# Kernel tuning notes

Measured on AMD Instinct MI355X. Metric: run time of the kernel, lower is better.

The kernel has to match this reference:

```python
import jax, jax.numpy as jnp
import numpy as np
from itertools import permutations

B, Nm, S, K, H, OUT = 32, 128, 16, 4, 128, 1
LG, LI, LGL = 3, 2, 2  # num_layer, num_layer_id, num_layer_global
EPS = 1e-5


def _ln(x, g, b):
    m = jnp.mean(x, -1, keepdims=True)
    v = jnp.mean(jnp.square(x - m), -1, keepdims=True)
    return (x - m) * jax.lax.rsqrt(v + EPS) * g + b


def _block(x, W1, b1, W2, b2, g, bn):
    # Linear -> ReLU -> Linear -> LayerNorm -> ReLU
    h = jax.nn.relu(x @ W1 + b1)
    return jax.nn.relu(_ln(h @ W2 + b2, g, bn))


def setup_inputs() -> dict:
    key = jax.random.key(0)
    ks = iter(jax.random.split(key, 64))
    nrm = lambda shape, s=0.05: jax.random.normal(next(ks), shape, jnp.float32) * s
    x = nrm((B, Nm, 1), 1.0)
    adj = (jax.random.uniform(next(ks), (B, Nm, Nm)) < 0.05).astype(jnp.float32)
    # allperm: all permutations of [1..K-1] with 0 prepended, transposed -> (K, permdim)
    ap = np.array(list(permutations(range(1, K))), dtype=np.int32)
    ap = np.concatenate([np.zeros((ap.shape[0], 1), np.int32), ap], axis=1).T
    allperm = jnp.asarray(ap)
    Ssub = B * S
    base = jax.random.randint(next(ks), (Ssub,), 0, Nm - K)
    subgs = base[:, None] + jnp.arange(K, dtype=jnp.int32)[None, :]  # distinct nodes per subgraph
    num_subg = jnp.full((B,), S, jnp.int32)
    num_node = jnp.full((B,), Nm, jnp.int32)
    d = dict(x=x, adj=adj,
             idemb=nrm((K + 2, H)),
             in_W1=nrm((1, H)), in_b1=jnp.zeros((H,)), in_W2=nrm((H, H)), in_b2=jnp.zeros((H,)),
             in_g=jnp.ones((H,)), in_bn=jnp.zeros((H,)),
             gW1=nrm((LG, H, H)), gb1=jnp.zeros((LG, H)), gW2=nrm((LG, H, H)), gb2=jnp.zeros((LG, H)),
             gg=jnp.ones((LG, H)), gbn=jnp.zeros((LG, H)),
             iW1=nrm((LI, H, H)), ib1=jnp.zeros((LI, H)), iW2=nrm((LI, H, H)), ib2=jnp.zeros((LI, H)),
             ig=jnp.ones((LI, H)), ibn=jnp.zeros((LI, H)),
             glW1=nrm((LGL, H, H)), glb1=jnp.zeros((LGL, H)), glW2=nrm((LGL, H, H)), glb2=jnp.zeros((LGL, H)),
             glg=jnp.ones((LGL, H)), glbn=jnp.zeros((LGL, H)),
             s1_W=nrm((H, H)), s1_b=jnp.zeros((H,)), s2_W=nrm((H, H)), s2_b=jnp.zeros((H,)),
             rW1=nrm((H, H)), rb1=jnp.zeros((H,)), rW2=nrm((H, H)), rb2=jnp.zeros((H,)),
             rg=jnp.ones((H,)), rbn=jnp.zeros((H,)),
             out_W=nrm((H, OUT)), out_b=jnp.zeros((OUT,)),
             subgs=subgs, num_subg=num_subg, num_node=num_node, allperm=allperm)
    return d


def reference(x, adj, idemb, in_W1, in_b1, in_W2, in_b2, in_g, in_bn,
              gW1, gb1, gW2, gb2, gg, gbn,
              iW1, ib1, iW2, ib2, ig, ibn,
              glW1, glb1, glW2, glb2, glg, glbn,
              s1_W, s1_b, s2_W, s2_b,
              rW1, rb1, rW2, rb2, rg, rbn,
              out_W, out_b, subgs, num_subg, num_node, allperm):
    Bsz, N = x.shape[0], x.shape[1]
    Ssub, k = subgs.shape
    permdim = allperm.shape[1]
    # input embedding MLP
    h = _block(x, in_W1, in_b1, in_W2, in_b2, in_g, in_bn)  # (B, Nm, H)
    Hd = h.shape[-1]
    # subgraph -> graph batch map (ns_b = S per graph; Ssub static)
    subgbatch = jnp.repeat(jnp.arange(Bsz), num_subg, total_repeat_length=Ssub)
    # identity labeling: z starts as ones, labeled nodes get idemb(allperm[pos])
    lb = jnp.repeat(jnp.arange(Ssub), k)          # label batch (subgraph idx)
    lnodes = subgs.reshape(-1)                    # node ids within graph
    ni = jnp.tile(jnp.arange(k), Ssub)            # position within subgraph
    vals = idemb[allperm[ni]]                     # (Ssub*k, permdim, H)
    z = jnp.ones((Ssub, N, permdim, Hd), x.dtype)
    z = z.at[lb, lnodes].multiply(vals)
    # graph message passing on full graphs
    for l in range(gW1.shape[0]):
        m = jnp.einsum('bij,bjd->bid', adj, h)
        h = h + _block(m, gW1[l], gb1[l], gW2[l], gb2[l], gg[l], gbn[l])
    hs = h[subgbatch]        # (Ssub, Nm, H)
    sadj = adj[subgbatch]    # (Ssub, Nm, Nm)
    # id message passing over permutation channels
    for l in range(iW1.shape[0]):
        m = jnp.einsum('bij,bjpd->bipd', sadj, z)
        z = z + _block(m, iW1[l], ib1[l], iW2[l], ib2[l], ig[l], ibn[l])
    # zero out padded (null) nodes
    null_mask = jnp.arange(N)[None, :] >= num_node[:, None]  # (B, Nm)
    z = jnp.where(null_mask[subgbatch][:, :, None, None], 0.0, z)
    z = jax.nn.relu(z.mean(axis=2) @ s1_W + s1_b)  # setmlp1, (Ssub, Nm, H)
    hs = hs + z
    for l in range(glW1.shape[0]):
        m = jnp.einsum('bij,bjd->bid', sadj, hs)
        hs = hs + _block(m, glW1[l], glb1[l], glW2[l], glb2[l], glg[l], glbn[l])
    hs = jax.nn.relu(hs.sum(axis=1) @ s2_W + s2_b)  # setmlp2, (Ssub, H)
    pooled = jax.ops.segment_max(hs, subgbatch, num_segments=Bsz)  # global max pool
    pooled = pooled + _block(pooled, rW1, rb1, rW2, rb2, rg, rbn)  # setmlp3 (1 layer)
    return pooled @ out_W + out_b  # (B, OUT)
```

## Files before the change

### kernel.cpp

```cpp
#include <hip/hip_runtime.h>
#include <hip/hip_bf16.h>
#include <string.h>

typedef __hip_bfloat16 bf16;
typedef short v8s __attribute__((ext_vector_type(8)));
typedef float v4f __attribute__((ext_vector_type(4)));

#define H_ 128
#define P_ 6
#define K_ 4
#define NBR_CAP 48

__device__ __forceinline__ float ldf(const float* p, size_t i) { return p[i]; }
__device__ __forceinline__ float ldf(const bf16* p, size_t i) { return __bfloat162float(p[i]); }

__device__ __forceinline__ float s2f(short s) {
    unsigned int u = ((unsigned int)(unsigned short)s) << 16;
    float f; __builtin_memcpy(&f, &u, 4); return f;
}
__device__ __forceinline__ short f2s(float v) {
    bf16 h = __float2bfloat16(v);
    short s; __builtin_memcpy(&s, &h, 2); return s;
}
__device__ __forceinline__ v4f MFMA(v8s a, v8s b, v4f c) {
    return __builtin_amdgcn_mfma_f32_16x16x32_bf16(a, b, c, 0, 0, 0);
}

__global__ __launch_bounds__(128) void k_csr(const float* __restrict__ adj,
    unsigned char* __restrict__ nbr, int* __restrict__ deg, float* __restrict__ degf)
{
    const int gi = blockIdx.x * 128 + threadIdx.x;
    const float* row = adj + (size_t)gi * 128;
    unsigned char* nb = nbr + (size_t)gi * NBR_CAP;
    int c = 0; float s = 0.f;
    for (int j = 0; j < 128; ++j) {
        float a = row[j];
        if (a != 0.f) { s += a; if (c < NBR_CAP) nb[c] = (unsigned char)j; ++c; }
    }
    deg[gi] = (c < NBR_CAP) ? c : NBR_CAP;
    degf[gi] = s;
}

__global__ __launch_bounds__(128) void k_adjb(const float* __restrict__ adj, bf16* __restrict__ adjb)
{
    const size_t i = (size_t)blockIdx.x * 128 + threadIdx.x;
    adjb[i] = __float2bfloat16(adj[i]);
}

__global__ __launch_bounds__(128) void k_wt8(
    const float* s0, const float* s1, const float* s2, const float* s3,
    const float* s4, const float* s5, const float* s6, const float* s7,
    bf16* __restrict__ dst)
{
    const int w = blockIdx.x >> 7, n = blockIdx.x & 127, k = threadIdx.x;
    const float* arr[8] = {s0, s1, s2, s3, s4, s5, s6, s7};
    dst[(size_t)w * 16384 + n * 128 + k] = __float2bfloat16(arr[w][k * 128 + n]);
}

__global__ __launch_bounds__(128) void k_wt1(const float* __restrict__ src, bf16* __restrict__ dst)
{
    const int n = blockIdx.x, k = threadIdx.x;
    dst[n * 128 + k] = __float2bfloat16(src[k * 128 + n]);
}

__global__ __launch_bounds__(128) void k_in_t1(const float* __restrict__ x,
    const float* __restrict__ W1, const float* __restrict__ b1, float* __restrict__ t1)
{
    int r = blockIdx.x, hd = threadIdx.x;
    t1[(size_t)r * H_ + hd] = fmaxf(fmaf(x[r], W1[hd], b1[hd]), 0.f);
}

template<bool DO_MM1, bool HAS_RES>
__global__ __launch_bounds__(128) void k_block(
    const float* __restrict__ in, const float* __restrict__ res, float* __restrict__ out,
    const float* __restrict__ W1, const float* __restrict__ b1,
    const float* __restrict__ W2, const float* __restrict__ b2,
    const float* __restrict__ gam, const float* __restrict__ bet)
{
    __shared__ float sA[16][136];
    __shared__ float sB[16][136];
    __shared__ float sStat[32];
    const int hd = threadIdx.x;
    const size_t row0 = (size_t)blockIdx.x * 16;
    #pragma unroll
    for (int r = 0; r < 16; ++r) sA[r][hd] = in[(row0 + r) * H_ + hd];
    __syncthreads();
    float acc[16];
    if (DO_MM1) {
        #pragma unroll
        for (int r = 0; r < 16; ++r) acc[r] = b1[hd];
        for (int k = 0; k < H_; k += 4) {
            float w0 = W1[(k+0)*H_+hd], w1 = W1[(k+1)*H_+hd], w2 = W1[(k+2)*H_+hd], w3 = W1[(k+3)*H_+hd];
            #pragma unroll
            for (int r = 0; r < 16; ++r) {
                float4 a = *(const float4*)&sA[r][k];
                acc[r] = fmaf(a.x, w0, acc[r]); acc[r] = fmaf(a.y, w1, acc[r]);
                acc[r] = fmaf(a.z, w2, acc[r]); acc[r] = fmaf(a.w, w3, acc[r]);
            }
        }
        #pragma unroll
        for (int r = 0; r < 16; ++r) sB[r][hd] = fmaxf(acc[r], 0.f);
    } else {
        #pragma unroll
        for (int r = 0; r < 16; ++r) sB[r][hd] = sA[r][hd];
    }
    __syncthreads();
    #pragma unroll
    for (int r = 0; r < 16; ++r) acc[r] = b2[hd];
    for (int k = 0; k < H_; k += 4) {
        float w0 = W2[(k+0)*H_+hd], w1 = W2[(k+1)*H_+hd], w2 = W2[(k+2)*H_+hd], w3 = W2[(k+3)*H_+hd];
        #pragma unroll
        for (int r = 0; r < 16; ++r) {
            float4 a = *(const float4*)&sB[r][k];
            acc[r] = fmaf(a.x, w0, acc[r]); acc[r] = fmaf(a.y, w1, acc[r]);
            acc[r] = fmaf(a.z, w2, acc[r]); acc[r] = fmaf(a.w, w3, acc[r]);
        }
    }
    __syncthreads();
    #pragma unroll
    for (int r = 0; r < 16; ++r) sA[r][hd] = acc[r];
    __syncthreads();
    if (hd < 16) {
        float s = 0.f, ss = 0.f;
        for (int k = 0; k < H_; ++k) { float v = sA[hd][k]; s += v; ss += v * v; }
        float mean = s * (1.f / H_);
        float var = ss * (1.f / H_) - mean * mean;
        sStat[hd] = mean; sStat[16 + hd] = rsqrtf(var + 1e-5f);
    }
    __syncthreads();
    float gv = gam[hd], bv = bet[hd];
    #pragma unroll
    for (int r = 0; r < 16; ++r) {
        float v = fmaxf((acc[r] - sStat[r]) * sStat[16 + r] * gv + bv, 0.f);
        if (HAS_RES) v += res[(row0 + r) * H_ + hd];
        out[(row0 + r) * H_ + hd] = v;
    }
}

template<bool GATHER, typename T>
__global__ __launch_bounds__(128) void k_gemm_relu(
    const T* __restrict__ in, const float* __restrict__ res, float* __restrict__ out,
    const float* __restrict__ W, const float* __restrict__ b)
{
    __shared__ float sA[16][136];
    const int hd = threadIdx.x;
    const size_t row0 = (size_t)blockIdx.x * 16;
    #pragma unroll
    for (int r = 0; r < 16; ++r) sA[r][hd] = ldf(in, (row0 + r) * H_ + hd);
    __syncthreads();
    float acc[16];
    #pragma unroll
    for (int r = 0; r < 16; ++r) acc[r] = b[hd];
    for (int k = 0; k < H_; k += 4) {
        float w0 = W[(k+0)*H_+hd], w1 = W[(k+1)*H_+hd], w2 = W[(k+2)*H_+hd], w3 = W[(k+3)*H_+hd];
        #pragma unroll
        for (int r = 0; r < 16; ++r) {
            float4 a = *(const float4*)&sA[r][k];
            acc[r] = fmaf(a.x, w0, acc[r]); acc[r] = fmaf(a.y, w1, acc[r]);
            acc[r] = fmaf(a.z, w2, acc[r]); acc[r] = fmaf(a.w, w3, acc[r]);
        }
    }
    #pragma unroll
    for (int r = 0; r < 16; ++r) {
        size_t rr = row0 + r;
        float v = fmaxf(acc[r], 0.f);
        if (GATHER) {
            int i = (int)(rr & 127);
            int g = (int)(rr >> 11);
            v += res[((size_t)(g * 128 + i)) * H_ + hd];
        }
        out[rr * H_ + hd] = v;
    }
}

__global__ __launch_bounds__(128) void k_spmv(const float* __restrict__ adj,
    const float* __restrict__ xin, float* __restrict__ mout, int subShift)
{
    __shared__ float sAdj[128];
    const int hd = threadIdx.x;
    const int bi = blockIdx.x;
    const int bb = bi >> 7, i = bi & 127;
    const int g = bb >> subShift;
    sAdj[hd] = adj[((size_t)(g * 128 + i)) * 128 + hd];
    __syncthreads();
    float acc = 0.f;
    const float* xb = xin + (size_t)bb * 128 * H_ + hd;
    for (int j = 0; j < 128; ++j) {
        float a = sAdj[j];
        if (a != 0.f) acc = fmaf(a, xb[(size_t)j * H_], acc);
    }
    mout[(size_t)bi * H_ + hd] = acc;
}

__global__ __launch_bounds__(256) void k_id1_fused(
    const float* __restrict__ adj, const float* __restrict__ degf,
    const int* __restrict__ subgs, const int* __restrict__ allperm,
    const float* __restrict__ idemb, bf16* __restrict__ outb,
    const bf16* __restrict__ W1t, const float* __restrict__ b1,
    const bf16* __restrict__ W2t, const float* __restrict__ b2,
    const float* __restrict__ gam, const float* __restrict__ bet)
{
    __shared__ __align__(16) short sIn[128][136];
    __shared__ __align__(16) short tb[4][32][136];
    __shared__ float sE[K_][128];
    const int t = threadIdx.x;
    const int bi = blockIdx.x;
    const int b_s = bi / 6, p = bi - b_s * 6;
    const int g = b_s >> 4;
    const int wave = t >> 6, lane = t & 63;
    const int quad = lane >> 4, l16 = lane & 15;

    int nodeq[K_];
    #pragma unroll
    for (int q = 0; q < K_; ++q) nodeq[q] = subgs[b_s * K_ + q];

    for (int u = t; u < K_ * 128; u += 256) {
        const int q = u >> 7, f = u & 127;
        sE[q][f] = idemb[(size_t)allperm[q * P_ + p] * H_ + f] - 1.f;
    }
    __syncthreads();

    {
        const int i = t >> 1, half = (t & 1) * 64;
        const int gi = g * 128 + i;
        const float dg = degf[gi];
        float aq[K_];
        #pragma unroll
        for (int q = 0; q < K_; ++q) aq[q] = adj[(size_t)gi * 128 + nodeq[q]];
        #pragma unroll
        for (int f = 0; f < 64; ++f) {
            float v = dg;
            #pragma unroll
            for (int q = 0; q < K_; ++q) v = fmaf(aq[q], sE[q][half + f], v);
            sIn[i][half + f] = f2s(v);
        }
    }
    __syncthreads();

    v4f acc[2][8];
    #pragma unroll
    for (int mt = 0; mt < 2; ++mt)
        #pragma unroll
        for (int nt = 0; nt < 8; ++nt) acc[mt][nt] = (v4f){0.f, 0.f, 0.f, 0.f};
    #pragma unroll
    for (int kk = 0; kk < 4; ++kk) {
        v8s a0 = *(const v8s*)&sIn[wave * 32 + l16][kk * 32 + quad * 8];
        v8s a1 = *(const v8s*)&sIn[wave * 32 + 16 + l16][kk * 32 + quad * 8];
        #pragma unroll
        for (int nt = 0; nt < 8; ++nt) {
            v8s b = *(const v8s*)(W1t + (nt * 16 + l16) * 128 + kk * 32 + quad * 8);
            acc[0][nt] = MFMA(a0, b, acc[0][nt]);
            acc[1][nt] = MFMA(a1, b, acc[1][nt]);
        }
    }
    #pragma unroll
    for (int nt = 0; nt < 8; ++nt) {
        float bb = b1[nt * 16 + l16];
        #pragma unroll
        for (int mt = 0; mt < 2; ++mt)
            #pragma unroll
            for (int r = 0; r < 4; ++r)
                tb[wave][mt * 16 + quad * 4 + r][nt * 16 + l16] = f2s(fmaxf(acc[mt][nt][r] + bb, 0.f));
    }
    #pragma unroll
    for (int mt = 0; mt < 2; ++mt)
        #pragma unroll
        for (int nt = 0; nt < 8; ++nt) acc[mt][nt] = (v4f){0.f, 0.f, 0.f, 0.f};
    #pragma unroll
    for (int kk = 0; kk < 4; ++kk) {
        v8s a0 = *(const v8s*)&tb[wave][l16][kk * 32 + quad * 8];
        v8s a1 = *(const v8s*)&tb[wave][16 + l16][kk * 32 + quad * 8];
        #pragma unroll
        for (int nt = 0; nt < 8; ++nt) {
            v8s b = *(const v8s*)(W2t + (nt * 16 + l16) * 128 + kk * 32 + quad * 8);
            acc[0][nt] = MFMA(a0, b, acc[0][nt]);
            acc[1][nt] = MFMA(a1, b, acc[1][nt]);
        }
    }
    float bb2[8], gv[8], bv[8];
    #pragma unroll
    for (int nt = 0; nt < 8; ++nt) {
        int n = nt * 16 + l16;
        bb2[nt] = b2[n]; gv[nt] = gam[n]; bv[nt] = bet[n];
    }
    #pragma unroll
    for (int mt = 0; mt < 2; ++mt)
        #pragma unroll
        for (int r = 0; r < 4; ++r) {
            float s = 0.f, q = 0.f;
            #pragma unroll
            for (int nt = 0; nt < 8; ++nt) {
                float u = acc[mt][nt][r] + bb2[nt];
                acc[mt][nt][r] = u;
                s += u; q += u * u;
            }
            #pragma unroll
            for (int d = 1; d < 16; d <<= 1) {
                s += __shfl_xor(s, d);
                q += __shfl_xor(q, d);
            }
            float mn = s * (1.f / 128.f);
            float rs = rsqrtf(q * (1.f / 128.f) - mn * mn + 1e-5f);
            #pragma unroll
            for (int nt = 0; nt < 8; ++nt) {
                float v = fmaxf((acc[mt][nt][r] - mn) * rs * gv[nt] + bv[nt], 0.f);
                tb[wave][mt * 16 + quad * 4 + r][nt * 16 + l16] = f2s(v + 1.0f);
            }
        }
    __syncthreads();
    {
        const int f = t >> 1, nh = (t & 1) * 64;
        const short* flat = &tb[0][0][0];
        bf16* dst = outb + (size_t)bi * 16384 + (size_t)f * 128 + nh;
        #pragma unroll
        for (int u = 0; u < 8; ++u) {
            v8s pk;
            #pragma unroll
            for (int e = 0; e < 8; ++e) pk[e] = flat[(nh + u * 8 + e) * 136 + f];
            *(v8s*)(dst + u * 8) = pk;
        }
    }
}

__global__ __launch_bounds__(256) void k_id2_v9(
    const bf16* __restrict__ z2t, bf16* __restrict__ zm,
    const bf16* __restrict__ adjb, const int* __restrict__ num_node,
    const int* __restrict__ subgs, const int* __restrict__ allperm,
    const float* __restrict__ idemb,
    const bf16* __restrict__ W1t, const float* __restrict__ b1,
    const bf16* __restrict__ W2t, const float* __restrict__ b2,
    const float* __restrict__ gam, const float* __restrict__ bet)
{
    __shared__ __align__(16) short sB[128][136];
    __shared__ float sP[4][128];
    const int t = threadIdx.x;
    const int b_s = blockIdx.x;
    const int g = b_s >> 4;
    const int wave = t >> 6, lane = t & 63, quad = lane >> 4, l16 = lane & 15;
    const int wrow = wave << 5;

    #pragma unroll
    for (int u = 0; u < 2; ++u) {
        const int v = t + u * 256;
        const int a = v >> 7, n = v & 127;
        const float* src = (a == 0) ? b1 : (a == 1) ? b2 : (a == 2) ? gam : bet;
        sP[a][n] = src[n];
    }

    v8s aA[2][4];
    {
        const bf16* ar = adjb + (size_t)g * 16384;
        #pragma unroll
        for (int mt = 0; mt < 2; ++mt)
            #pragma unroll
            for (int kk = 0; kk < 4; ++kk)
                aA[mt][kk] = *(const v8s*)(ar + (size_t)(wrow + mt * 16 + l16) * 128 + kk * 32 + quad * 8);
    }
    int nodeq[K_];
    #pragma unroll
    for (int q = 0; q < K_; ++q) nodeq[q] = subgs[b_s * K_ + q];

    float macc[2][8][4];
    #pragma unroll
    for (int mt = 0; mt < 2; ++mt)
        #pragma unroll
        for (int nt = 0; nt < 8; ++nt)
            #pragma unroll
            for (int r = 0; r < 4; ++r) macc[mt][nt][r] = 0.f;

    const int sf = t >> 1, shalf = (t & 1) * 64;

    for (int p = 0; p < P_; ++p) {
        {
            const bf16* src = z2t + ((size_t)(b_s * P_ + p)) * 16384 + (size_t)sf * 128 + shalf;
            #pragma unroll
            for (int u = 0; u < 8; ++u)
                *(v8s*)&sB[sf][shalf + u * 8] = *(const v8s*)(src + u * 8);
        }
        __syncthreads();
        if (t < 128) {
            #pragma unroll
            for (int q = 0; q < K_; ++q) {
                float e = idemb[(size_t)allperm[q * P_ + p] * H_ + t] - 1.f;
                short* cell = &sB[t][nodeq[q]];
                *cell = f2s(s2f(*cell) + e);
            }
        }
        __syncthreads();
        #pragma unroll
        for (int mt = 0; mt < 2; ++mt)
            #pragma unroll
            for (int nt = 0; nt < 8; ++nt) {
                const int n = nt * 16 + l16;
                #pragma unroll
                for (int r = 0; r < 4; ++r)
                    macc[mt][nt][r] += s2f(sB[n][wrow + mt * 16 + quad * 4 + r]);
            }
        v4f acc[2][8];
        #pragma unroll
        for (int mt = 0; mt < 2; ++mt)
            #pragma unroll
            for (int nt = 0; nt < 8; ++nt) acc[mt][nt] = (v4f){0.f, 0.f, 0.f, 0.f};
        #pragma unroll
        for (int kk = 0; kk < 4; ++kk)
            #pragma unroll
            for (int nt = 0; nt < 8; ++nt) {
                v8s b = *(const v8s*)&sB[nt * 16 + l16][kk * 32 + quad * 8];
                acc[0][nt] = MFMA(aA[0][kk], b, acc[0][nt]);
                acc[1][nt] = MFMA(aA[1][kk], b, acc[1][nt]);
            }
        __syncthreads();
        #pragma unroll
        for (int nt = 0; nt < 8; ++nt)
            #pragma unroll
            for (int mt = 0; mt < 2; ++mt)
                #pragma unroll
                for (int r = 0; r < 4; ++r)
                    sB[wrow + mt * 16 + quad * 4 + r][nt * 16 + l16] = f2s(acc[mt][nt][r]);
        #pragma unroll
        for (int mt = 0; mt < 2; ++mt)
            #pragma unroll
            for (int nt = 0; nt < 8; ++nt) acc[mt][nt] = (v4f){0.f, 0.f, 0.f, 0.f};
        #pragma unroll
        for (int kk = 0; kk < 4; ++kk) {
            v8s a0 = *(const v8s*)&sB[wrow + l16][kk * 32 + quad * 8];
            v8s a1 = *(const v8s*)&sB[wrow + 16 + l16][kk * 32 + quad * 8];
            #pragma unroll
            for (int nt = 0; nt < 8; ++nt) {
                v8s b = *(const v8s*)(W1t + (nt * 16 + l16) * 128 + kk * 32 + quad * 8);
                acc[0][nt] = MFMA(a0, b, acc[0][nt]);
                acc[1][nt] = MFMA(a1, b, acc[1][nt]);
            }
        }
        #pragma unroll
        for (int nt = 0; nt < 8; ++nt) {
            float bb = sP[0][nt * 16 + l16];
            #pragma unroll
            for (int mt = 0; mt < 2; ++mt)
                #pragma unroll
                for (int r = 0; r < 4; ++r)
                    sB[wrow + mt * 16 + quad * 4 + r][nt * 16 + l16] = f2s(fmaxf(acc[mt][nt][r] + bb, 0.f));
        }
        #pragma unroll
        for (int mt = 0; mt < 2; ++mt)
            #pragma unroll
            for (int nt = 0; nt < 8; ++nt) acc[mt][nt] = (v4f){0.f, 0.f, 0.f, 0.f};
        #pragma unroll
        for (int kk = 0; kk < 4; ++kk) {
            v8s a0 = *(const v8s*)&sB[wrow + l16][kk * 32 + quad * 8];
            v8s a1 = *(const v8s*)&sB[wrow + 16 + l16][kk * 32 + quad * 8];
            #pragma unroll
            for (int nt = 0; nt < 8; ++nt) {
                v8s b = *(const v8s*)(W2t + (nt * 16 + l16) * 128 + kk * 32 + quad * 8);
                acc[0][nt] = MFMA(a0, b, acc[0][nt]);
                acc[1][nt] = MFMA(a1, b, acc[1][nt]);
            }
        }
        #pragma unroll
        for (int mt = 0; mt < 2; ++mt)
            #pragma unroll
            for (int r = 0; r < 4; ++r) {
                float s = 0.f, qq = 0.f;
                #pragma unroll
                for (int nt = 0; nt < 8; ++nt) {
                    float u = acc[mt][nt][r] + sP[1][nt * 16 + l16];
                    acc[mt][nt][r] = u;
                    s += u; qq += u * u;
                }
                #pragma unroll
                for (int d = 1; d < 16; d <<= 1) {
                    s += __shfl_xor(s, d);
                    qq += __shfl_xor(qq, d);
                }
                float mn = s * (1.f / 128.f);
                float rs = rsqrtf(qq * (1.f / 128.f) - mn * mn + 1e-5f);
                #pragma unroll
                for (int nt = 0; nt < 8; ++nt) {
                    const int n = nt * 16 + l16;
                    macc[mt][nt][r] += fmaxf((acc[mt][nt][r] - mn) * rs * sP[2][n] + sP[3][n], 0.f);
                }
            }
        __syncthreads();
    }
    const int nn = num_node[g];
    #pragma unroll
    for (int mt = 0; mt < 2; ++mt)
        #pragma unroll
        for (int nt = 0; nt < 8; ++nt)
            #pragma unroll
            for (int r = 0; r < 4; ++r) {
                const int i = wrow + mt * 16 + quad * 4 + r;
                const int n = nt * 16 + l16;
                float v = (i >= nn) ? 0.f : macc[mt][nt][r] * (1.f / 6.f);
                zm[((size_t)(b_s * 128 + i)) * 128 + n] = __float2bfloat16(v);
            }
}

__global__ __launch_bounds__(256) void k_gl_fused(
    const bf16* __restrict__ zm, const float* __restrict__ hb,
    const bf16* __restrict__ adjb,
    const bf16* __restrict__ s1Wt, const float* __restrict__ s1_b,
    const bf16* __restrict__ WTgl,
    const float* __restrict__ glb1, const float* __restrict__ glb2,
    const float* __restrict__ glg, const float* __restrict__ glbn,
    float* __restrict__ hsum)
{
    __shared__ __align__(16) short sHsT[128][136];
    __shared__ __align__(16) short sM[128][136];
    __shared__ float sP[9][128];
    const int t = threadIdx.x;
    const int b_s = blockIdx.x;
    const int g = b_s >> 4;
    const int wave = t >> 6, lane = t & 63, quad = lane >> 4, l16 = lane & 15;
    const int wrow = wave << 5;

    for (int u = t; u < 9 * 128; u += 256) {
        const int a = u >> 7, n = u & 127;
        const float* src =
            (a == 0) ? glb1 : (a == 1) ? glb2 : (a == 2) ? glg : (a == 3) ? glbn :
            (a == 4) ? glb1 + 128 : (a == 5) ? glb2 + 128 : (a == 6) ? glg + 128 :
            (a == 7) ? glbn + 128 : s1_b;
        sP[a][n] = src[n];
    }

    v8s aA[2][4];
    {
        const bf16* ar = adjb + (size_t)g * 16384;
        #pragma unroll
        for (int mt = 0; mt < 2; ++mt)
            #pragma unroll
            for (int kk = 0; kk < 4; ++kk)
                aA[mt][kk] = *(const v8s*)(ar + (size_t)(wrow + mt * 16 + l16) * 128 + kk * 32 + quad * 8);
    }

    v4f acc[2][8];
    #pragma unroll
    for (int mt = 0; mt < 2; ++mt)
        #pragma unroll
        for (int nt = 0; nt < 8; ++nt) acc[mt][nt] = (v4f){0.f, 0.f, 0.f, 0.f};
    #pragma unroll
    for (int kk = 0; kk < 4; ++kk) {
        v8s a0 = *(const v8s*)(zm + ((size_t)(b_s * 128) + wrow + l16) * 128 + kk * 32 + quad * 8);
        v8s a1 = *(const v8s*)(zm + ((size_t)(b_s * 128) + wrow + 16 + l16) * 128 + kk * 32 + quad * 8);
        #pragma unroll
        for (int nt = 0; nt < 8; ++nt) {
            v8s b = *(const v8s*)(s1Wt + (nt * 16 + l16) * 128 + kk * 32 + quad * 8);
            acc[0][nt] = MFMA(a0, b, acc[0][nt]);
            acc[1][nt] = MFMA(a1, b, acc[1][nt]);
        }
    }
    __syncthreads();
    float hs_reg[2][8][4];
    #pragma unroll
    for (int mt = 0; mt < 2; ++mt)
        #pragma unroll
        for (int nt = 0; nt < 8; ++nt)
            #pragma unroll
            for (int r = 0; r < 4; ++r) {
                const int i = wrow + mt * 16 + quad * 4 + r;
                const int n = nt * 16 + l16;
                float v = fmaxf(acc[mt][nt][r] + sP[8][n], 0.f);
                v += hb[((size_t)(g * 128 + i)) * 128 + n];
                hs_reg[mt][nt][r] = v;
                sHsT[n][i] = f2s(v);
            }
    __syncthreads();

    for (int l = 0; l < 2; ++l) {
        const bf16* W1t = WTgl + (size_t)(2 * l) * 16384;
        const bf16* W2t = WTgl + (size_t)(2 * l + 1) * 16384;
        #pragma unroll
        for (int mt = 0; mt < 2; ++mt)
            #pragma unroll
            for (int nt = 0; nt < 8; ++nt) acc[mt][nt] = (v4f){0.f, 0.f, 0.f, 0.f};
        #pragma unroll
        for (int kk = 0; kk < 4; ++kk)
            #pragma unroll
            for (int nt = 0; nt < 8; ++nt) {
                v8s b = *(const v8s*)&sHsT[nt * 16 + l16][kk * 32 + quad * 8];
                acc[0][nt] = MFMA(aA[0][kk], b, acc[0][nt]);
                acc[1][nt] = MFMA(aA[1][kk], b, acc[1][nt]);
            }
        #pragma unroll
        for (int nt = 0; nt < 8; ++nt)
            #pragma unroll
            for (int mt = 0; mt < 2; ++mt)
                #pragma unroll
                for (int r = 0; r < 4; ++r)
                    sM[wrow + mt * 16 + quad * 4 + r][nt * 16 + l16] = f2s(acc[mt][nt][r]);
        __syncthreads();
        #pragma unroll
        for (int mt = 0; mt < 2; ++mt)
            #pragma unroll
            for (int nt = 0; nt < 8; ++nt) acc[mt][nt] = (v4f){0.f, 0.f, 0.f, 0.f};
        #pragma unroll
        for (int kk = 0; kk < 4; ++kk) {
            v8s a0 = *(const v8s*)&sM[wrow + l16][kk * 32 + quad * 8];
            v8s a1 = *(const v8s*)&sM[wrow + 16 + l16][kk * 32 + quad * 8];
            #pragma unroll
            for (int nt = 0; nt < 8; ++nt) {
                v8s b = *(const v8s*)(W1t + (nt * 16 + l16) * 128 + kk * 32 + quad * 8);
                acc[0][nt] = MFMA(a0, b, acc[0][nt]);
                acc[1][nt] = MFMA(a1, b, acc[1][nt]);
            }
        }
        #pragma unroll
        for (int nt = 0; nt < 8; ++nt) {
            float bb = sP[4 * l + 0][nt * 16 + l16];
            #pragma unroll
            for (int mt = 0; mt < 2; ++mt)
                #pragma unroll
                for (int r = 0; r < 4; ++r)
                    sM[wrow + mt * 16 + quad * 4 + r][nt * 16 + l16] = f2s(fmaxf(acc[mt][nt][r] + bb, 0.f));
        }
        #pragma unroll
        for (int mt = 0; mt < 2; ++mt)
            #pragma unroll
            for (int nt = 0; nt < 8; ++nt) acc[mt][nt] = (v4f){0.f, 0.f, 0.f, 0.f};
        #pragma unroll
        for (int kk = 0; kk < 4; ++kk) {
            v8s a0 = *(const v8s*)&sM[wrow + l16][kk * 32 + quad * 8];
            v8s a1 = *(const v8s*)&sM[wrow + 16 + l16][kk * 32 + quad * 8];
            #pragma unroll
            for (int nt = 0; nt < 8; ++nt) {
                v8s b = *(const v8s*)(W2t + (nt * 16 + l16) * 128 + kk * 32 + quad * 8);
                acc[0][nt] = MFMA(a0, b, acc[0][nt]);
                acc[1][nt] = MFMA(a1, b, acc[1][nt]);
            }
        }
        #pragma unroll
        for (int mt = 0; mt < 2; ++mt)
            #pragma unroll
            for (int r = 0; r < 4; ++r) {
                float s = 0.f, qq = 0.f;
                #pragma unroll
                for (int nt = 0; nt < 8; ++nt) {
                    float u = acc[mt][nt][r] + sP[4 * l + 1][nt * 16 + l16];
                    acc[mt][nt][r] = u;
                    s += u; qq += u * u;
                }
                #pragma unroll
                for (int d = 1; d < 16; d <<= 1) {
                    s += __shfl_xor(s, d);
                    qq += __shfl_xor(qq, d);
                }
                float mn = s * (1.f / 128.f);
                float rs = rsqrtf(qq * (1.f / 128.f) - mn * mn + 1e-5f);
                const int i = wrow + mt * 16 + quad * 4 + r;
                #pragma unroll
                for (int nt = 0; nt < 8; ++nt) {
                    const int n = nt * 16 + l16;
                    float v = fmaxf((acc[mt][nt][r] - mn) * rs * sP[4 * l + 2][n] + sP[4 * l + 3][n], 0.f);
                    float h2 = hs_reg[mt][nt][r] + v;
                    hs_reg[mt][nt][r] = h2;
                    sHsT[n][i] = f2s(h2);
                }
            }
        __syncthreads();
    }

    float* sRedf = (float*)&sM[0][0];
    #pragma unroll
    for (int nt = 0; nt < 8; ++nt) {
        float part = 0.f;
        #pragma unroll
        for (int mt = 0; mt < 2; ++mt)
            #pragma unroll
            for (int r = 0; r < 4; ++r) part += hs_reg[mt][nt][r];
        sRedf[(wave * 4 + quad) * 128 + nt * 16 + l16] = part;
    }
    __syncthreads();
    if (t < 128) {
        float s = 0.f;
        #pragma unroll
        for (int r = 0; r < 16; ++r) s += sRedf[r * 128 + t];
        hsum[(size_t)b_s * 128 + t] = s;
    }
}

__global__ __launch_bounds__(128) void k_maxpool(const float* __restrict__ hs2, float* __restrict__ pooled)
{
    const int g = blockIdx.x, hd = threadIdx.x;
    float m = -INFINITY;
    for (int s = 0; s < 16; ++s) m = fmaxf(m, hs2[((size_t)(g * 16 + s)) * H_ + hd]);
    pooled[(size_t)g * H_ + hd] = m;
}

__global__ __launch_bounds__(128) void k_out(const float* __restrict__ pooled2,
    const float* __restrict__ out_W, const float* __restrict__ out_b, float* __restrict__ out)
{
    __shared__ float red[128];
    const int g = blockIdx.x, hd = threadIdx.x;
    red[hd] = pooled2[(size_t)g * H_ + hd] * out_W[hd];
    __syncthreads();
    for (int s = 64; s > 0; s >>= 1) {
        if (hd < s) red[hd] += red[hd + s];
        __syncthreads();
    }
    if (hd == 0) out[g] = red[0] + out_b[0];
}

extern "C" void kernel_launch(void* const* d_in, const int* in_sizes, int n_in,
                              void* d_out, int out_size, void* d_ws, size_t ws_size,
                              hipStream_t stream)
{
    (void)in_sizes; (void)n_in; (void)out_size; (void)ws_size;
    const float* x     = (const float*)d_in[0];
    const float* adj   = (const float*)d_in[1];
    const float* idemb = (const float*)d_in[2];
    const float* in_W1 = (const float*)d_in[3];
    const float* in_b1 = (const float*)d_in[4];
    const float* in_W2 = (const float*)d_in[5];
    const float* in_b2 = (const float*)d_in[6];
    const float* in_g  = (const float*)d_in[7];
    const float* in_bn = (const float*)d_in[8];
    const float* gW1   = (const float*)d_in[9];
    const float* gb1   = (const float*)d_in[10];
    const float* gW2   = (const float*)d_in[11];
    const float* gb2   = (const float*)d_in[12];
    const float* gg    = (const float*)d_in[13];
    const float* gbn   = (const float*)d_in[14];
    const float* iW1   = (const float*)d_in[15];
    const float* ib1   = (const float*)d_in[16];
    const float* iW2   = (const float*)d_in[17];
    const float* ib2   = (const float*)d_in[18];
    const float* ig    = (const float*)d_in[19];
    const float* ibn   = (const float*)d_in[20];
    const float* glW1  = (const float*)d_in[21];
    const float* glb1  = (const float*)d_in[22];
    const float* glW2  = (const float*)d_in[23];
    const float* glb2  = (const float*)d_in[24];
    const float* glg   = (const float*)d_in[25];
    const float* glbn  = (const float*)d_in[26];
    const float* s1_W  = (const float*)d_in[27];
    const float* s1_b  = (const float*)d_in[28];
    const float* s2_W  = (const float*)d_in[29];
    const float* s2_b  = (const float*)d_in[30];
    const float* rW1   = (const float*)d_in[31];
    const float* rb1   = (const float*)d_in[32];
    const float* rW2   = (const float*)d_in[33];
    const float* rb2   = (const float*)d_in[34];
    const float* rg    = (const float*)d_in[35];
    const float* rbn   = (const float*)d_in[36];
    const float* out_W = (const float*)d_in[37];
    const float* out_b = (const float*)d_in[38];
    const int* subgs   = (const int*)d_in[39];
    const int* num_node= (const int*)d_in[41];
    const int* allperm = (const int*)d_in[42];

    const size_t MB_ = (size_t)512 * 128 * P_ * H_ * 2;
    char* w = (char*)d_ws;
    bf16*  mz     = (bf16*)(w);
    bf16*  s1Wt   = (bf16*)(w + 33554432ull);
    bf16*  zm     = (bf16*)(w + MB_);
    bf16*  WT     = (bf16*)(w + MB_ + 16777216ull);
    char*  wc     = w + MB_ + 16777216ull + 262144ull;
    float* hb     = (float*)(wc);
    float* sb2    = (float*)(wc + 2097152ull);
    bf16*  adjb   = (bf16*)(wc + 2097152ull);
    float* hsum   = (float*)(wc + 4194304ull);
    float* hs2    = (float*)(wc + 4456448ull);
    float* pooled = (float*)(wc + 4718592ull);
    float* pooled2= (float*)(wc + 4734976ull);
    unsigned char* nbr = (unsigned char*)(wc + 4751360ull);
    int*   deg    = (int*)(wc + 4947968ull);
    float* degf   = (float*)(wc + 4964352ull);
    float* outp   = (float*)d_out;

    k_csr<<<32, 128, 0, stream>>>(adj, nbr, deg, degf);
    k_wt8<<<1024, 128, 0, stream>>>(iW1, iW2, iW1 + 16384, iW2 + 16384,
                                    glW1, glW2, glW1 + 16384, glW2 + 16384, WT);

    k_in_t1<<<4096, 128, 0, stream>>>(x, in_W1, in_b1, sb2);
    k_block<false, false><<<256, 128, 0, stream>>>(sb2, nullptr, hb,
        nullptr, nullptr, in_W2, in_b2, in_g, in_bn);

    for (int l = 0; l < 3; ++l) {
        k_spmv<<<4096, 128, 0, stream>>>(adj, hb, sb2, 0);
        k_block<true, true><<<256, 128, 0, stream>>>(sb2, hb, hb,
            gW1 + l * 16384, gb1 + l * 128, gW2 + l * 16384, gb2 + l * 128,
            gg + l * 128, gbn + l * 128);
    }

    k_adjb<<<4096, 128, 0, stream>>>(adj, adjb);

    k_id1_fused<<<3072, 256, 0, stream>>>(adj, degf, subgs, allperm, idemb, mz,
        WT, ib1, WT + 16384, ib2, ig, ibn);

    k_id2_v9<<<512, 256, 0, stream>>>(mz, zm, adjb, num_node, subgs, allperm, idemb,
        WT + 2 * 16384, ib1 + 128, WT + 3 * 16384, ib2 + 128, ig + 128, ibn + 128);

    k_wt1<<<128, 128, 0, stream>>>(s1_W, s1Wt);

    k_gl_fused<<<512, 256, 0, stream>>>(zm, hb, adjb, s1Wt, s1_b,
        WT + 4 * 16384, glb1, glb2, glg, glbn, hsum);

    k_gemm_relu<false, float><<<32, 128, 0, stream>>>(hsum, nullptr, hs2, s2_W, s2_b);
    k_maxpool<<<32, 128, 0, stream>>>(hs2, pooled);
    k_block<true, true><<<2, 128, 0, stream>>>(pooled, pooled, pooled2,
        rW1, rb1, rW2, rb2, rg, rbn);
    k_out<<<32, 128, 0, stream>>>(pooled2, out_W, out_b, outp);
}
```

Measured before the change: 685.6 us.

## Fuse id-layer-1 and id-layer-2 kernels to keep permutation activations on-chip

Merges the first id message-passing layer kernel into the second, so each subgraph block computes the layer-1 input, both MLP GEMMs and layernorm per permutation, then writes the transposed result into shared memory for layer 2. This removes a large bf16 intermediate buffer (about 100MB written and read back) and one kernel launch. In exchange, grid parallelism drops from 3072 to 512 blocks with a serial loop over six permutations, and each block does more work and synchronisation.

```diff
diff --git a/kernel.cpp b/kernel.cpp
--- a/kernel.cpp
+++ b/kernel.cpp
@@ -4,6 +4,7 @@
 
 typedef __hip_bfloat16 bf16;
 typedef short v8s __attribute__((ext_vector_type(8)));
+typedef short v4s __attribute__((ext_vector_type(4)));
 typedef float v4f __attribute__((ext_vector_type(4)));
 
 #define H_ 128
@@ -192,147 +193,18 @@
     mout[(size_t)bi * H_ + hd] = acc;
 }
 
-__global__ __launch_bounds__(256) void k_id1_fused(
+__global__ __launch_bounds__(256) void k_id12(
     const float* __restrict__ adj, const float* __restrict__ degf,
-    const int* __restrict__ subgs, const int* __restrict__ allperm,
-    const float* __restrict__ idemb, bf16* __restrict__ outb,
-    const bf16* __restrict__ W1t, const float* __restrict__ b1,
-    const bf16* __restrict__ W2t, const float* __restrict__ b2,
-    const float* __restrict__ gam, const float* __restrict__ bet)
-{
-    __shared__ __align__(16) short sIn[128][136];
-    __shared__ __align__(16) short tb[4][32][136];
-    __shared__ float sE[K_][128];
-    const int t = threadIdx.x;
-    const int bi = blockIdx.x;
-    const int b_s = bi / 6, p = bi - b_s * 6;
-    const int g = b_s >> 4;
-    const int wave = t >> 6, lane = t & 63;
-    const int quad = lane >> 4, l16 = lane & 15;
-
-    int nodeq[K_];
-    #pragma unroll
-    for (int q = 0; q < K_; ++q) nodeq[q] = subgs[b_s * K_ + q];
-
-    for (int u = t; u < K_ * 128; u += 256) {
-        const int q = u >> 7, f = u & 127;
-        sE[q][f] = idemb[(size_t)allperm[q * P_ + p] * H_ + f] - 1.f;
-    }
-    __syncthreads();
-
-    {
-        const int i = t >> 1, half = (t & 1) * 64;
-        const int gi = g * 128 + i;
-        const float dg = degf[gi];
-        float aq[K_];
-        #pragma unroll
-        for (int q = 0; q < K_; ++q) aq[q] = adj[(size_t)gi * 128 + nodeq[q]];
-        #pragma unroll
-        for (int f = 0; f < 64; ++f) {
-            float v = dg;
-            #pragma unroll
-            for (int q = 0; q < K_; ++q) v = fmaf(aq[q], sE[q][half + f], v);
-            sIn[i][half + f] = f2s(v);
-        }
-    }
-    __syncthreads();
-
-    v4f acc[2][8];
-    #pragma unroll
-    for (int mt = 0; mt < 2; ++mt)
-        #pragma unroll
-        for (int nt = 0; nt < 8; ++nt) acc[mt][nt] = (v4f){0.f, 0.f, 0.f, 0.f};
-    #pragma unroll
-    for (int kk = 0; kk < 4; ++kk) {
-        v8s a0 = *(const v8s*)&sIn[wave * 32 + l16][kk * 32 + quad * 8];
-        v8s a1 = *(const v8s*)&sIn[wave * 32 + 16 + l16][kk * 32 + quad * 8];
-        #pragma unroll
-        for (int nt = 0; nt < 8; ++nt) {
-            v8s b = *(const v8s*)(W1t + (nt * 16 + l16) * 128 + kk * 32 + quad * 8);
-            acc[0][nt] = MFMA(a0, b, acc[0][nt]);
-            acc[1][nt] = MFMA(a1, b, acc[1][nt]);
-        }
-    }
-    #pragma unroll
-    for (int nt = 0; nt < 8; ++nt) {
-        float bb = b1[nt * 16 + l16];
-        #pragma unroll
-        for (int mt = 0; mt < 2; ++mt)
-            #pragma unroll
-            for (int r = 0; r < 4; ++r)
-                tb[wave][mt * 16 + quad * 4 + r][nt * 16 + l16] = f2s(fmaxf(acc[mt][nt][r] + bb, 0.f));
-    }
-    #pragma unroll
-    for (int mt = 0; mt < 2; ++mt)
-        #pragma unroll
-        for (int nt = 0; nt < 8; ++nt) acc[mt][nt] = (v4f){0.f, 0.f, 0.f, 0.f};
-    #pragma unroll
-    for (int kk = 0; kk < 4; ++kk) {
-        v8s a0 = *(const v8s*)&tb[wave][l16][kk * 32 + quad * 8];
-        v8s a1 = *(const v8s*)&tb[wave][16 + l16][kk * 32 + quad * 8];
-        #pragma unroll
-        for (int nt = 0; nt < 8; ++nt) {
-            v8s b = *(const v8s*)(W2t + (nt * 16 + l16) * 128 + kk * 32 + quad * 8);
-            acc[0][nt] = MFMA(a0, b, acc[0][nt]);
-            acc[1][nt] = MFMA(a1, b, acc[1][nt]);
-        }
-    }
-    float bb2[8], gv[8], bv[8];
-    #pragma unroll
-    for (int nt = 0; nt < 8; ++nt) {
-        int n = nt * 16 + l16;
-        bb2[nt] = b2[n]; gv[nt] = gam[n]; bv[nt] = bet[n];
-    }
-    #pragma unroll
-    for (int mt = 0; mt < 2; ++mt)
-        #pragma unroll
-        for (int r = 0; r < 4; ++r) {
-            float s = 0.f, q = 0.f;
-            #pragma unroll
-            for (int nt = 0; nt < 8; ++nt) {
-                float u = acc[mt][nt][r] + bb2[nt];
-                acc[mt][nt][r] = u;
-                s += u; q += u * u;
-            }
-            #pragma unroll
-            for (int d = 1; d < 16; d <<= 1) {
-                s += __shfl_xor(s, d);
-                q += __shfl_xor(q, d);
-            }
-            float mn = s * (1.f / 128.f);
-            float rs = rsqrtf(q * (1.f / 128.f) - mn * mn + 1e-5f);
-            #pragma unroll
-            for (int nt = 0; nt < 8; ++nt) {
-                float v = fmaxf((acc[mt][nt][r] - mn) * rs * gv[nt] + bv[nt], 0.f);
-                tb[wave][mt * 16 + quad * 4 + r][nt * 16 + l16] = f2s(v + 1.0f);
-            }
-        }
-    __syncthreads();
-    {
-        const int f = t >> 1, nh = (t & 1) * 64;
-        const short* flat = &tb[0][0][0];
-        bf16* dst = outb + (size_t)bi * 16384 + (size_t)f * 128 + nh;
-        #pragma unroll
-        for (int u = 0; u < 8; ++u) {
-            v8s pk;
-            #pragma unroll
-            for (int e = 0; e < 8; ++e) pk[e] = flat[(nh + u * 8 + e) * 136 + f];
-            *(v8s*)(dst + u * 8) = pk;
-        }
-    }
-}
-
-__global__ __launch_bounds__(256) void k_id2_v9(
-    const bf16* __restrict__ z2t, bf16* __restrict__ zm,
     const bf16* __restrict__ adjb, const int* __restrict__ num_node,
     const int* __restrict__ subgs, const int* __restrict__ allperm,
-    const float* __restrict__ idemb,
-    const bf16* __restrict__ W1t, const float* __restrict__ b1,
-    const bf16* __restrict__ W2t, const float* __restrict__ b2,
-    const float* __restrict__ gam, const float* __restrict__ bet)
+    const float* __restrict__ idemb, bf16* __restrict__ zm,
+    const bf16* __restrict__ WT,
+    const float* __restrict__ ib1, const float* __restrict__ ib2,
+    const float* __restrict__ ig, const float* __restrict__ ibn)
 {
     __shared__ __align__(16) short sB[128][136];
-    __shared__ float sP[4][128];
+    __shared__ float sP[8][128];
+    __shared__ float sE[K_][128];
     const int t = threadIdx.x;
     const int b_s = blockIdx.x;
     const int g = b_s >> 4;
@@ -340,10 +212,12 @@
     const int wrow = wave << 5;
 
     #pragma unroll
-    for (int u = 0; u < 2; ++u) {
+    for (int u = 0; u < 4; ++u) {
         const int v = t + u * 256;
         const int a = v >> 7, n = v & 127;
-        const float* src = (a == 0) ? b1 : (a == 1) ? b2 : (a == 2) ? gam : bet;
+        const float* src = (a == 0) ? ib1 : (a == 1) ? ib2 : (a == 2) ? ig : (a == 3) ? ibn
+                         : (a == 4) ? ib1 + 128 : (a == 5) ? ib2 + 128
+                         : (a == 6) ? ig + 128 : ibn + 128;
         sP[a][n] = src[n];
     }
 
@@ -360,6 +234,13 @@
     #pragma unroll
     for (int q = 0; q < K_; ++q) nodeq[q] = subgs[b_s * K_ + q];
 
+    const int mi = t >> 1, mhalf = (t & 1) * 64;
+    const int gmi = g * 128 + mi;
+    const float dg = degf[gmi];
+    float aqm[K_];
+    #pragma unroll
+    for (int q = 0; q < K_; ++q) aqm[q] = adj[(size_t)gmi * 128 + nodeq[q]];
+
     float macc[2][8][4];
     #pragma unroll
     for (int mt = 0; mt < 2; ++mt)
@@ -368,35 +249,106 @@
             #pragma unroll
             for (int r = 0; r < 4; ++r) macc[mt][nt][r] = 0.f;
 
-    const int sf = t >> 1, shalf = (t & 1) * 64;
-
     for (int p = 0; p < P_; ++p) {
-        {
-            const bf16* src = z2t + ((size_t)(b_s * P_ + p)) * 16384 + (size_t)sf * 128 + shalf;
-            #pragma unroll
-            for (int u = 0; u < 8; ++u)
-                *(v8s*)&sB[sf][shalf + u * 8] = *(const v8s*)(src + u * 8);
+        for (int u = t; u < K_ * 128; u += 256) {
+            const int q = u >> 7, f = u & 127;
+            sE[q][f] = idemb[(size_t)allperm[q * P_ + p] * H_ + f] - 1.f;
         }
         __syncthreads();
-        if (t < 128) {
-            #pragma unroll
-            for (int q = 0; q < K_; ++q) {
-                float e = idemb[(size_t)allperm[q * P_ + p] * H_ + t] - 1.f;
-                short* cell = &sB[t][nodeq[q]];
-                *cell = f2s(s2f(*cell) + e);
-            }
-        }
+        #pragma unroll
+        for (int fb = 0; fb < 64; fb += 8) {
+            v8s pk;
+            #pragma unroll
+            for (int e = 0; e < 8; ++e) {
+                float v = dg;
+                #pragma unroll
+                for (int q = 0; q < K_; ++q) v = fmaf(aqm[q], sE[q][mhalf + fb + e], v);
+                pk[e] = f2s(v);
+            }
+            *(v8s*)&sB[mi][mhalf + fb] = pk;
+        }
+        v4f acc[2][8];
+        #pragma unroll
+        for (int mt = 0; mt < 2; ++mt)
+            #pragma unroll
+            for (int nt = 0; nt < 8; ++nt) acc[mt][nt] = (v4f){0.f, 0.f, 0.f, 0.f};
+        #pragma unroll
+        for (int kk = 0; kk < 4; ++kk) {
+            v8s a0 = *(const v8s*)&sB[wrow + l16][kk * 32 + quad * 8];
+            v8s a1 = *(const v8s*)&sB[wrow + 16 + l16][kk * 32 + quad * 8];
+            #pragma unroll
+            for (int nt = 0; nt < 8; ++nt) {
+                v8s b = *(const v8s*)(WT + (nt * 16 + l16) * 128 + kk * 32 + quad * 8);
+                acc[0][nt] = MFMA(a0, b, acc[0][nt]);
+                acc[1][nt] = MFMA(a1, b, acc[1][nt]);
+            }
+        }
+        #pragma unroll
+        for (int nt = 0; nt < 8; ++nt) {
+            float bb = sP[0][nt * 16 + l16];
+            #pragma unroll
+            for (int mt = 0; mt < 2; ++mt)
+                #pragma unroll
+                for (int r = 0; r < 4; ++r)
+                    sB[wrow + mt * 16 + quad * 4 + r][nt * 16 + l16] = f2s(fmaxf(acc[mt][nt][r] + bb, 0.f));
+        }
+        #pragma unroll
+        for (int mt = 0; mt < 2; ++mt)
+            #pragma unroll
+            for (int nt = 0; nt < 8; ++nt) acc[mt][nt] = (v4f){0.f, 0.f, 0.f, 0.f};
+        #pragma unroll
+        for (int kk = 0; kk < 4; ++kk) {
+            v8s a0 = *(const v8s*)&sB[wrow + l16][kk * 32 + quad * 8];
+            v8s a1 = *(const v8s*)&sB[wrow + 16 + l16][kk * 32 + quad * 8];
+            #pragma unroll
+            for (int nt = 0; nt < 8; ++nt) {
+                v8s b = *(const v8s*)(WT + 16384 + (nt * 16 + l16) * 128 + kk * 32 + quad * 8);
+                acc[0][nt] = MFMA(a0, b, acc[0][nt]);
+                acc[1][nt] = MFMA(a1, b, acc[1][nt]);
+            }
+        }
+        v4s zs[2][8];
+        #pragma unroll
+        for (int mt = 0; mt < 2; ++mt)
+            #pragma unroll
+            for (int r = 0; r < 4; ++r) {
+                float s = 0.f, qq = 0.f;
+                #pragma unroll
+                for (int nt = 0; nt < 8; ++nt) {
+                    float u = acc[mt][nt][r] + sP[1][nt * 16 + l16];
+                    acc[mt][nt][r] = u;
+                    s += u; qq += u * u;
+                }
+                #pragma unroll
+                for (int d = 1; d < 16; d <<= 1) {
+                    s += __shfl_xor(s, d);
+                    qq += __shfl_xor(qq, d);
+                }
+                float mn = s * (1.f / 128.f);
+                float rs = rsqrtf(qq * (1.f / 128.f) - mn * mn + 1e-5f);
+                const int i = wrow + mt * 16 + quad * 4 + r;
+                int eq = -1;
+                #pragma unroll
+                for (int q = 0; q < K_; ++q) if (nodeq[q] == i) eq = q;
+                #pragma unroll
+                for (int nt = 0; nt < 8; ++nt) {
+                    const int n = nt * 16 + l16;
+                    float v = fmaxf((acc[mt][nt][r] - mn) * rs * sP[2][n] + sP[3][n], 0.f);
+                    short z = f2s(v + 1.0f);
+                    if (eq >= 0) z = f2s(s2f(z) + sE[eq][n]);
+                    macc[mt][nt][r] += s2f(z);
+                    zs[mt][nt][r] = z;
+                }
+            }
         __syncthreads();
         #pragma unroll
-        for (int mt = 0; mt < 2; ++mt)
-            #pragma unroll
-            for (int nt = 0; nt < 8; ++nt) {
-                const int n = nt * 16 + l16;
-                #pragma unroll
-                for (int r = 0; r < 4; ++r)
-                    macc[mt][nt][r] += s2f(sB[n][wrow + mt * 16 + quad * 4 + r]);
-            }
-        v4f acc[2][8];
+        for (int mt = 0; mt < 2; ++mt) {
+            const int i0 = wrow + mt * 16 + quad * 4;
+            #pragma unroll
+            for (int nt = 0; nt < 8; ++nt)
+                *(v4s*)&sB[nt * 16 + l16][i0] = zs[mt][nt];
+        }
+        __syncthreads();
         #pragma unroll
         for (int mt = 0; mt < 2; ++mt)
             #pragma unroll
@@ -427,14 +379,14 @@
             v8s a1 = *(const v8s*)&sB[wrow + 16 + l16][kk * 32 + quad * 8];
             #pragma unroll
             for (int nt = 0; nt < 8; ++nt) {
-                v8s b = *(const v8s*)(W1t + (nt * 16 + l16) * 128 + kk * 32 + quad * 8);
+                v8s b = *(const v8s*)(WT + 2 * 16384 + (nt * 16 + l16) * 128 + kk * 32 + quad * 8);
                 acc[0][nt] = MFMA(a0, b, acc[0][nt]);
                 acc[1][nt] = MFMA(a1, b, acc[1][nt]);
             }
         }
         #pragma unroll
         for (int nt = 0; nt < 8; ++nt) {
-            float bb = sP[0][nt * 16 + l16];
+            float bb = sP[4][nt * 16 + l16];
             #pragma unroll
             for (int mt = 0; mt < 2; ++mt)
                 #pragma unroll
@@ -451,7 +403,7 @@
             v8s a1 = *(const v8s*)&sB[wrow + 16 + l16][kk * 32 + quad * 8];
             #pragma unroll
             for (int nt = 0; nt < 8; ++nt) {
-                v8s b = *(const v8s*)(W2t + (nt * 16 + l16) * 128 + kk * 32 + quad * 8);
+                v8s b = *(const v8s*)(WT + 3 * 16384 + (nt * 16 + l16) * 128 + kk * 32 + quad * 8);
                 acc[0][nt] = MFMA(a0, b, acc[0][nt]);
                 acc[1][nt] = MFMA(a1, b, acc[1][nt]);
             }
@@ -463,7 +415,7 @@
                 float s = 0.f, qq = 0.f;
                 #pragma unroll
                 for (int nt = 0; nt < 8; ++nt) {
-                    float u = acc[mt][nt][r] + sP[1][nt * 16 + l16];
+                    float u = acc[mt][nt][r] + sP[5][nt * 16 + l16];
                     acc[mt][nt][r] = u;
                     s += u; qq += u * u;
                 }
@@ -477,10 +429,9 @@
                 #pragma unroll
                 for (int nt = 0; nt < 8; ++nt) {
                     const int n = nt * 16 + l16;
-                    macc[mt][nt][r] += fmaxf((acc[mt][nt][r] - mn) * rs * sP[2][n] + sP[3][n], 0.f);
-                }
-            }
-        __syncthreads();
+                    macc[mt][nt][r] += fmaxf((acc[mt][nt][r] - mn) * rs * sP[6][n] + sP[7][n], 0.f);
+                }
+            }
     }
     const int nn = num_node[g];
     #pragma unroll
@@ -750,7 +701,6 @@
 
     const size_t MB_ = (size_t)512 * 128 * P_ * H_ * 2;
     char* w = (char*)d_ws;
-    bf16*  mz     = (bf16*)(w);
     bf16*  s1Wt   = (bf16*)(w + 33554432ull);
     bf16*  zm     = (bf16*)(w + MB_);
     bf16*  WT     = (bf16*)(w + MB_ + 16777216ull);
@@ -784,11 +734,8 @@
 
     k_adjb<<<4096, 128, 0, stream>>>(adj, adjb);
 
-    k_id1_fused<<<3072, 256, 0, stream>>>(adj, degf, subgs, allperm, idemb, mz,
-        WT, ib1, WT + 16384, ib2, ig, ibn);
-
-    k_id2_v9<<<512, 256, 0, stream>>>(mz, zm, adjb, num_node, subgs, allperm, idemb,
-        WT + 2 * 16384, ib1 + 128, WT + 3 * 16384, ib2 + 128, ig + 128, ibn + 128);
+    k_id12<<<512, 256, 0, stream>>>(adj, degf, adjb, num_node, subgs, allperm, idemb, zm,
+        WT, ib1, ib2, ig, ibn);
 
     k_wt1<<<128, 128, 0, stream>>>(s1_W, s1Wt);
 
```

Result: slower. 958.7 us (+39.8%).
